# Kernel tuning notes

Hardware: AMD Instinct MI355X
Metric: run time of the kernel (lower is better)

## Reference

```python
import jax, jax.numpy as jnp
import numpy as np

N = 65536
EMB_DIM = 1024
PICK_NUM = 12  # ceil(ln(65536)) = ceil(11.09) = 12


def setup_inputs() -> dict:
    key = jax.random.key(0)
    k_emb, k_wq, k_bq, k_wk, k_bk, k_idx = jax.random.split(key, 6)
    s = 1.0 / np.sqrt(EMB_DIM)
    embed_matrix = jax.random.normal(k_emb, (N, EMB_DIM), dtype=jnp.float32)
    Wq = jax.random.normal(k_wq, (EMB_DIM, EMB_DIM), dtype=jnp.float32) * s
    bq = jax.random.normal(k_bq, (EMB_DIM,), dtype=jnp.float32) * s
    Wk = jax.random.normal(k_wk, (EMB_DIM, EMB_DIM), dtype=jnp.float32) * s
    bk = jax.random.normal(k_bk, (EMB_DIM,), dtype=jnp.float32) * s
    # np.random.choice(n, pick_num, replace=False) -> deterministic permutation slice
    indices = jax.random.permutation(k_idx, N)[:PICK_NUM].astype(jnp.int32)
    return {"embed_matrix": embed_matrix, "Wq": Wq, "bq": bq,
            "Wk": Wk, "bk": bk, "indices": indices}


def reference(embed_matrix, Wq, bq, Wk, bk, indices):
    pick_num = indices.shape[0]
    # torch.nn.Linear: y = x @ W.T + b
    query = embed_matrix @ Wq.T + bq          # [n, d]
    key = embed_matrix @ Wk.T + bk            # [n, d]
    new_key = key[indices]                    # [pick, d] sampled keys
    Q_K_sample = query @ new_key.T            # [n, pick]
    max_values = jnp.max(Q_K_sample, axis=1)  # [n]
    _, top_indices = jax.lax.top_k(max_values, pick_num)
    Q_reduced = query[top_indices]            # [pick, d]
    Q_K = Q_reduced @ key.T                   # [pick, n]
    pooled = jnp.max(Q_K, axis=0, keepdims=True)  # [1, n]
    attention_embed = pooled @ embed_matrix   # [1, d]
    return attention_embed
```

## Files before the change

### kernel.cpp

```cpp
#include <hip/hip_runtime.h>

#define DIM 1024
#define NROWS 65536
#define PICK 12


__global__ void __launch_bounds__(256)
rows12_kernel(const float* __restrict__ emb, const float* __restrict__ W,
              const float* __restrict__ b, const int* __restrict__ idx,
              float* __restrict__ out) {
    int d = blockIdx.x;
    int t = threadIdx.x;
    int lane = t & 63;
    int q = t >> 6;
    int e0 = q * 256 + lane * 4;
    float4 w4 = *(const float4*)&W[(size_t)d * DIM + e0];
    float part[PICK];
#pragma unroll
    for (int j = 0; j < PICK; ++j) {
        int r = idx[j];
        float4 e4 = *(const float4*)&emb[(size_t)r * DIM + e0];
        part[j] = w4.x * e4.x + w4.y * e4.y + w4.z * e4.z + w4.w * e4.w;
    }
#pragma unroll
    for (int j = 0; j < PICK; ++j) {
        float v = part[j];
        for (int s = 32; s > 0; s >>= 1) v += __shfl_down(v, s, 64);
        part[j] = v;
    }
    __shared__ float red[4][PICK];
    if (lane == 0) {
#pragma unroll
        for (int j = 0; j < PICK; ++j) red[q][j] = part[j];
    }
    __syncthreads();
    if (t < PICK) {
        float s = red[0][t] + red[1][t] + red[2][t] + red[3][t] + b[d];
        out[t * DIM + d] = s;
    }
}

__global__ void __launch_bounds__(256)
colmat_kernel(const float* __restrict__ W, const float* __restrict__ V,
              const float* __restrict__ b, float* __restrict__ out,
              float* __restrict__ cvec) {
    int blk = blockIdx.x;
    int t = threadIdx.x;
    if (blk == 128) {
        float part[PICK];
#pragma unroll
        for (int j = 0; j < PICK; ++j) part[j] = 0.f;
        for (int k = 0; k < 4; ++k) {
            int d = t + k * 256;
            float bv = b[d];
#pragma unroll
            for (int j = 0; j < PICK; ++j) part[j] += bv * V[j * DIM + d];
        }
#pragma unroll
        for (int j = 0; j < PICK; ++j) {
            float v = part[j];
            for (int s = 32; s > 0; s >>= 1) v += __shfl_down(v, s, 64);
            if ((t & 63) == 0) atomicAdd(&cvec[j], v);
        }
        return;
    }
    int eg = blk & 3;
    int dg = blk >> 2;
    int e = eg * 256 + t;
    int d0 = dg * 32;
    __shared__ float Vs[PICK][32];
    for (int i = t; i < PICK * 32; i += 256) {
        int j = i >> 5, dd = i & 31;
        Vs[j][dd] = V[j * DIM + d0 + dd];
    }
    __syncthreads();
    float acc[PICK];
#pragma unroll
    for (int j = 0; j < PICK; ++j) acc[j] = 0.f;
    for (int dd = 0; dd < 32; ++dd) {
        float w = W[(size_t)(d0 + dd) * DIM + e];
#pragma unroll
        for (int j = 0; j < PICK; ++j) acc[j] += w * Vs[j][dd];
    }
#pragma unroll
    for (int j = 0; j < PICK; ++j) atomicAdd(&out[e * PICK + j], acc[j]);
}


__global__ void __launch_bounds__(256)
pass1_kernel(const float* __restrict__ emb, const float* __restrict__ M,
             const float* __restrict__ c0, float* __restrict__ maxv) {
    __shared__ float sM[DIM * PICK];
    int t = threadIdx.x;
    for (int i = t; i < DIM * PICK / 4; i += 256)
        ((float4*)sM)[i] = ((const float4*)M)[i];
    __syncthreads();

    int l = t & 63, w = t >> 6;
    int g = l >> 2, s = l & 3;
    size_t wbase = (size_t)blockIdx.x * 256 + w * 64;
    const float* rp[4];
    float4 cur[4];
#pragma unroll
    for (int rr = 0; rr < 4; ++rr) {
        rp[rr] = emb + (wbase + rr * 16 + g) * DIM + s * 4;
        cur[rr] = *(const float4*)rp[rr];
    }
    float cb[PICK];
#pragma unroll
    for (int j = 0; j < PICK; ++j) cb[j] = c0[j];

    float acc[4][PICK];
#pragma unroll
    for (int rr = 0; rr < 4; ++rr)
#pragma unroll
        for (int j = 0; j < PICK; ++j) acc[rr][j] = 0.f;

    for (int i = 0; i < 64; ++i) {
        int ip = (i + 1 < 64) ? i + 1 : i;
        float4 nxt[4];
#pragma unroll
        for (int rr = 0; rr < 4; ++rr) nxt[rr] = *(const float4*)(rp[rr] + ip * 16);
        const float* mb = sM + (size_t)(i * 16 + s * 4) * PICK;
        float4 m[12];
#pragma unroll
        for (int k = 0; k < 12; ++k) m[k] = *(const float4*)(mb + k * 4);
#pragma unroll
        for (int rr = 0; rr < 4; ++rr) {
            float f[4] = {cur[rr].x, cur[rr].y, cur[rr].z, cur[rr].w};
#pragma unroll
            for (int x = 0; x < 4; ++x) {
                float4 a0 = m[3 * x], a1 = m[3 * x + 1], a2 = m[3 * x + 2];
                acc[rr][0] += f[x] * a0.x; acc[rr][1] += f[x] * a0.y;
                acc[rr][2] += f[x] * a0.z; acc[rr][3] += f[x] * a0.w;
                acc[rr][4] += f[x] * a1.x; acc[rr][5] += f[x] * a1.y;
                acc[rr][6] += f[x] * a1.z; acc[rr][7] += f[x] * a1.w;
                acc[rr][8] += f[x] * a2.x; acc[rr][9] += f[x] * a2.y;
                acc[rr][10] += f[x] * a2.z; acc[rr][11] += f[x] * a2.w;
            }
        }
#pragma unroll
        for (int rr = 0; rr < 4; ++rr) cur[rr] = nxt[rr];
    }
#pragma unroll
    for (int rr = 0; rr < 4; ++rr)
#pragma unroll
        for (int j = 0; j < PICK; ++j) {
            acc[rr][j] += __shfl_xor(acc[rr][j], 1, 64);
            acc[rr][j] += __shfl_xor(acc[rr][j], 2, 64);
        }
    float mx[4];
#pragma unroll
    for (int rr = 0; rr < 4; ++rr) {
        float v = acc[rr][0] + cb[0];
#pragma unroll
        for (int j = 1; j < PICK; ++j) v = fmaxf(v, acc[rr][j] + cb[j]);
        mx[rr] = v;
    }
    float sel = (s == 0) ? mx[0] : (s == 1) ? mx[1] : (s == 2) ? mx[2] : mx[3];
    maxv[wbase + s * 16 + g] = sel;
}

__global__ void __launch_bounds__(256)
pass2_kernel(const float* __restrict__ emb, const float* __restrict__ Rt,
             const float* __restrict__ c1, float* __restrict__ out) {
    __shared__ float sM[DIM * PICK];
    __shared__ float pooled[256];
    int t = threadIdx.x;
    for (int i = t; i < DIM * PICK / 4; i += 256)
        ((float4*)sM)[i] = ((const float4*)Rt)[i];
    __syncthreads();

    int l = t & 63, w = t >> 6;
    int g = l >> 2, s = l & 3;
    size_t bbase = (size_t)blockIdx.x * 256;
    size_t wbase = bbase + w * 64;
    const float* rp[4];
    float4 cur[4];
#pragma unroll
    for (int rr = 0; rr < 4; ++rr) {
        rp[rr] = emb + (wbase + rr * 16 + g) * DIM + s * 4;
        cur[rr] = *(const float4*)rp[rr];
    }
    float cb[PICK];
#pragma unroll
    for (int j = 0; j < PICK; ++j) cb[j] = c1[j];

    float acc[4][PICK];
#pragma unroll
    for (int rr = 0; rr < 4; ++rr)
#pragma unroll
        for (int j = 0; j < PICK; ++j) acc[rr][j] = 0.f;

    for (int i = 0; i < 64; ++i) {
        int ip = (i + 1 < 64) ? i + 1 : i;
        float4 nxt[4];
#pragma unroll
        for (int rr = 0; rr < 4; ++rr) nxt[rr] = *(const float4*)(rp[rr] + ip * 16);
        const float* mb = sM + (size_t)(i * 16 + s * 4) * PICK;
        float4 m[12];
#pragma unroll
        for (int k = 0; k < 12; ++k) m[k] = *(const float4*)(mb + k * 4);
#pragma unroll
        for (int rr = 0; rr < 4; ++rr) {
            float f[4] = {cur[rr].x, cur[rr].y, cur[rr].z, cur[rr].w};
#pragma unroll
            for (int x = 0; x < 4; ++x) {
                float4 a0 = m[3 * x], a1 = m[3 * x + 1], a2 = m[3 * x + 2];
                acc[rr][0] += f[x] * a0.x; acc[rr][1] += f[x] * a0.y;
                acc[rr][2] += f[x] * a0.z; acc[rr][3] += f[x] * a0.w;
                acc[rr][4] += f[x] * a1.x; acc[rr][5] += f[x] * a1.y;
                acc[rr][6] += f[x] * a1.z; acc[rr][7] += f[x] * a1.w;
                acc[rr][8] += f[x] * a2.x; acc[rr][9] += f[x] * a2.y;
                acc[rr][10] += f[x] * a2.z; acc[rr][11] += f[x] * a2.w;
            }
        }
#pragma unroll
        for (int rr = 0; rr < 4; ++rr) cur[rr] = nxt[rr];
    }
#pragma unroll
    for (int rr = 0; rr < 4; ++rr)
#pragma unroll
        for (int j = 0; j < PICK; ++j) {
            acc[rr][j] += __shfl_xor(acc[rr][j], 1, 64);
            acc[rr][j] += __shfl_xor(acc[rr][j], 2, 64);
        }
    float mx[4];
#pragma unroll
    for (int rr = 0; rr < 4; ++rr) {
        float v = acc[rr][0] + cb[0];
#pragma unroll
        for (int j = 1; j < PICK; ++j) v = fmaxf(v, acc[rr][j] + cb[j]);
        mx[rr] = v;
    }
    float sel = (s == 0) ? mx[0] : (s == 1) ? mx[1] : (s == 2) ? mx[2] : mx[3];
    pooled[w * 64 + s * 16 + g] = sel;
    __syncthreads();

    const float* tp = emb + bbase * DIM + t * 4;
    float4 o = {0.f, 0.f, 0.f, 0.f};
#pragma unroll 8
    for (int r = 0; r < 256; ++r) {
        float p = pooled[r];
        float4 v = *(const float4*)(tp + (size_t)r * DIM);
        o.x += p * v.x; o.y += p * v.y; o.z += p * v.z; o.w += p * v.w;
    }
    atomicAdd(&out[t * 4 + 0], o.x);
    atomicAdd(&out[t * 4 + 1], o.y);
    atomicAdd(&out[t * 4 + 2], o.z);
    atomicAdd(&out[t * 4 + 3], o.w);
}

__global__ void __launch_bounds__(256)
top12_local(const float* __restrict__ maxv, float* __restrict__ cand_v,
            int* __restrict__ cand_i) {
    int t = threadIdx.x;
    int base = blockIdx.x * 1024;
    __shared__ float mv[1024];
    __shared__ float sv[256];
    __shared__ int si[256];
    for (int i = t; i < 1024; i += 256) mv[i] = maxv[base + i];
    __syncthreads();
    for (int k = 0; k < PICK; ++k) {
        float bv = -3e38f; int bi = 0x7fffffff;
        for (int i = t; i < 1024; i += 256) {
            float v = mv[i];
            if (v > bv || (v == bv && base + i < bi)) { bv = v; bi = base + i; }
        }
        sv[t] = bv; si[t] = bi;
        __syncthreads();
        for (int s = 128; s > 0; s >>= 1) {
            if (t < s) {
                if (sv[t + s] > sv[t] || (sv[t + s] == sv[t] && si[t + s] < si[t])) {
                    sv[t] = sv[t + s]; si[t] = si[t + s];
                }
            }
            __syncthreads();
        }
        if (t == 0) {
            cand_v[blockIdx.x * PICK + k] = sv[0];
            cand_i[blockIdx.x * PICK + k] = si[0];
            mv[si[0] - base] = -3e38f;
        }
        __syncthreads();
    }
}

__global__ void __launch_bounds__(256)
top12_merge(const float* __restrict__ cand_v, const int* __restrict__ cand_i,
            int* __restrict__ top_idx) {
    int t = threadIdx.x;
    __shared__ float mv[768];
    __shared__ int mi[768];
    __shared__ float sv[256];
    __shared__ int si[256];
    __shared__ int sl[256];
    for (int i = t; i < 768; i += 256) { mv[i] = cand_v[i]; mi[i] = cand_i[i]; }
    __syncthreads();
    for (int k = 0; k < PICK; ++k) {
        float bv = -3e38f; int bi = 0x7fffffff; int bl = -1;
        for (int i = t; i < 768; i += 256) {
            float v = mv[i]; int ii = mi[i];
            if (v > bv || (v == bv && ii < bi)) { bv = v; bi = ii; bl = i; }
        }
        sv[t] = bv; si[t] = bi; sl[t] = bl;
        __syncthreads();
        for (int s = 128; s > 0; s >>= 1) {
            if (t < s) {
                if (sv[t + s] > sv[t] || (sv[t + s] == sv[t] && si[t + s] < si[t])) {
                    sv[t] = sv[t + s]; si[t] = si[t + s]; sl[t] = sl[t + s];
                }
            }
            __syncthreads();
        }
        if (t == 0) { top_idx[k] = si[0]; mv[sl[0]] = -3e38f; }
        __syncthreads();
    }
}

extern "C" void kernel_launch(void* const* d_in, const int* in_sizes, int n_in,
                              void* d_out, int out_size, void* d_ws, size_t ws_size,
                              hipStream_t stream) {
    const float* emb = (const float*)d_in[0];
    const float* Wq  = (const float*)d_in[1];
    const float* bq  = (const float*)d_in[2];
    const float* Wk  = (const float*)d_in[3];
    const float* bk  = (const float*)d_in[4];
    const int* indices = (const int*)d_in[5];
    float* out = (float*)d_out;
    float* ws = (float*)d_ws;

    float* NK      = ws;
    float* Qr      = ws + 12288;
    float* M       = ws + 24576;
    float* Rt      = ws + 36864;
    float* c0      = ws + 49152;
    float* c1      = ws + 49168;
    float* cand_v  = ws + 49184;
    int*   cand_i  = (int*)(ws + 49952);
    int*   top_idx = (int*)(ws + 50720);
    float* maxv    = ws + 50736;

    hipMemsetAsync(M, 0, (size_t)(12288 * 2 + 32) * sizeof(float), stream);
    hipMemsetAsync(out, 0, DIM * sizeof(float), stream);

    rows12_kernel<<<1024, 256, 0, stream>>>(emb, Wk, bk, indices, NK);
    colmat_kernel<<<129, 256, 0, stream>>>(Wq, NK, bq, M, c0);
    pass1_kernel<<<256, 256, 0, stream>>>(emb, M, c0, maxv);
    top12_local<<<64, 256, 0, stream>>>(maxv, cand_v, cand_i);
    top12_merge<<<1, 256, 0, stream>>>(cand_v, cand_i, top_idx);
    rows12_kernel<<<1024, 256, 0, stream>>>(emb, Wq, bq, top_idx, Qr);
    colmat_kernel<<<129, 256, 0, stream>>>(Wk, Qr, bk, Rt, c1);
    pass2_kernel<<<256, 256, 0, stream>>>(emb, Rt, c1, out);
}
```

Baseline: 605.9 us.

## Halve rows per block in streaming passes, deepen prefetch, use wave-level top-k

pass1 and pass2 now give each block 128 rows instead of 256, launch twice as many blocks, and request two resident blocks per CU. They also prefetch two iterations ahead instead of one. The aim is to spread the 256 MB embedding stream over all CUs, since 256 blocks underfills a 256-CU part, and to hide more memory latency. The top-12 local and merge kernels are rewritten as single-wavefront register and shuffle reductions, which removes the shared-memory tree and its barriers. The cost is more per-block shared-memory reloads of the 48 KB matrix and twice as many output atomics in pass2.

```diff
diff --git a/kernel.cpp b/kernel.cpp
--- a/kernel.cpp
+++ b/kernel.cpp
@@ -87,7 +87,7 @@
 }
 
 
-__global__ void __launch_bounds__(256)
+__global__ void __launch_bounds__(256, 2)
 pass1_kernel(const float* __restrict__ emb, const float* __restrict__ M,
              const float* __restrict__ c0, float* __restrict__ maxv) {
     __shared__ float sM[DIM * PICK];
@@ -98,35 +98,36 @@
 
     int l = t & 63, w = t >> 6;
     int g = l >> 2, s = l & 3;
-    size_t wbase = (size_t)blockIdx.x * 256 + w * 64;
-    const float* rp[4];
-    float4 cur[4];
-#pragma unroll
-    for (int rr = 0; rr < 4; ++rr) {
+    size_t wbase = (size_t)blockIdx.x * 128 + w * 32;
+    const float* rp[2];
+    float4 cur[2], nxt[2];
+#pragma unroll
+    for (int rr = 0; rr < 2; ++rr) {
         rp[rr] = emb + (wbase + rr * 16 + g) * DIM + s * 4;
         cur[rr] = *(const float4*)rp[rr];
+        nxt[rr] = *(const float4*)(rp[rr] + 16);
     }
     float cb[PICK];
 #pragma unroll
     for (int j = 0; j < PICK; ++j) cb[j] = c0[j];
 
-    float acc[4][PICK];
-#pragma unroll
-    for (int rr = 0; rr < 4; ++rr)
+    float acc[2][PICK];
+#pragma unroll
+    for (int rr = 0; rr < 2; ++rr)
 #pragma unroll
         for (int j = 0; j < PICK; ++j) acc[rr][j] = 0.f;
 
     for (int i = 0; i < 64; ++i) {
-        int ip = (i + 1 < 64) ? i + 1 : i;
-        float4 nxt[4];
-#pragma unroll
-        for (int rr = 0; rr < 4; ++rr) nxt[rr] = *(const float4*)(rp[rr] + ip * 16);
+        int ip2 = (i + 2 < 64) ? i + 2 : 63;
+        float4 n2[2];
+#pragma unroll
+        for (int rr = 0; rr < 2; ++rr) n2[rr] = *(const float4*)(rp[rr] + ip2 * 16);
         const float* mb = sM + (size_t)(i * 16 + s * 4) * PICK;
         float4 m[12];
 #pragma unroll
         for (int k = 0; k < 12; ++k) m[k] = *(const float4*)(mb + k * 4);
 #pragma unroll
-        for (int rr = 0; rr < 4; ++rr) {
+        for (int rr = 0; rr < 2; ++rr) {
             float f[4] = {cur[rr].x, cur[rr].y, cur[rr].z, cur[rr].w};
 #pragma unroll
             for (int x = 0; x < 4; ++x) {
@@ -140,32 +141,31 @@
             }
         }
 #pragma unroll
-        for (int rr = 0; rr < 4; ++rr) cur[rr] = nxt[rr];
-    }
-#pragma unroll
-    for (int rr = 0; rr < 4; ++rr)
+        for (int rr = 0; rr < 2; ++rr) { cur[rr] = nxt[rr]; nxt[rr] = n2[rr]; }
+    }
+#pragma unroll
+    for (int rr = 0; rr < 2; ++rr)
 #pragma unroll
         for (int j = 0; j < PICK; ++j) {
             acc[rr][j] += __shfl_xor(acc[rr][j], 1, 64);
             acc[rr][j] += __shfl_xor(acc[rr][j], 2, 64);
         }
-    float mx[4];
-#pragma unroll
-    for (int rr = 0; rr < 4; ++rr) {
+    float mx[2];
+#pragma unroll
+    for (int rr = 0; rr < 2; ++rr) {
         float v = acc[rr][0] + cb[0];
 #pragma unroll
         for (int j = 1; j < PICK; ++j) v = fmaxf(v, acc[rr][j] + cb[j]);
         mx[rr] = v;
     }
-    float sel = (s == 0) ? mx[0] : (s == 1) ? mx[1] : (s == 2) ? mx[2] : mx[3];
-    maxv[wbase + s * 16 + g] = sel;
-}
-
-__global__ void __launch_bounds__(256)
+    if (s < 2) maxv[wbase + s * 16 + g] = (s == 0) ? mx[0] : mx[1];
+}
+
+__global__ void __launch_bounds__(256, 2)
 pass2_kernel(const float* __restrict__ emb, const float* __restrict__ Rt,
              const float* __restrict__ c1, float* __restrict__ out) {
     __shared__ float sM[DIM * PICK];
-    __shared__ float pooled[256];
+    __shared__ float pooled[128];
     int t = threadIdx.x;
     for (int i = t; i < DIM * PICK / 4; i += 256)
         ((float4*)sM)[i] = ((const float4*)Rt)[i];
@@ -173,36 +173,37 @@
 
     int l = t & 63, w = t >> 6;
     int g = l >> 2, s = l & 3;
-    size_t bbase = (size_t)blockIdx.x * 256;
-    size_t wbase = bbase + w * 64;
-    const float* rp[4];
-    float4 cur[4];
-#pragma unroll
-    for (int rr = 0; rr < 4; ++rr) {
+    size_t bbase = (size_t)blockIdx.x * 128;
+    size_t wbase = bbase + w * 32;
+    const float* rp[2];
+    float4 cur[2], nxt[2];
+#pragma unroll
+    for (int rr = 0; rr < 2; ++rr) {
         rp[rr] = emb + (wbase + rr * 16 + g) * DIM + s * 4;
         cur[rr] = *(const float4*)rp[rr];
+        nxt[rr] = *(const float4*)(rp[rr] + 16);
     }
     float cb[PICK];
 #pragma unroll
     for (int j = 0; j < PICK; ++j) cb[j] = c1[j];
 
-    float acc[4][PICK];
-#pragma unroll
-    for (int rr = 0; rr < 4; ++rr)
+    float acc[2][PICK];
+#pragma unroll
+    for (int rr = 0; rr < 2; ++rr)
 #pragma unroll
         for (int j = 0; j < PICK; ++j) acc[rr][j] = 0.f;
 
     for (int i = 0; i < 64; ++i) {
-        int ip = (i + 1 < 64) ? i + 1 : i;
-        float4 nxt[4];
-#pragma unroll
-        for (int rr = 0; rr < 4; ++rr) nxt[rr] = *(const float4*)(rp[rr] + ip * 16);
+        int ip2 = (i + 2 < 64) ? i + 2 : 63;
+        float4 n2[2];
+#pragma unroll
+        for (int rr = 0; rr < 2; ++rr) n2[rr] = *(const float4*)(rp[rr] + ip2 * 16);
         const float* mb = sM + (size_t)(i * 16 + s * 4) * PICK;
         float4 m[12];
 #pragma unroll
         for (int k = 0; k < 12; ++k) m[k] = *(const float4*)(mb + k * 4);
 #pragma unroll
-        for (int rr = 0; rr < 4; ++rr) {
+        for (int rr = 0; rr < 2; ++rr) {
             float f[4] = {cur[rr].x, cur[rr].y, cur[rr].z, cur[rr].w};
 #pragma unroll
             for (int x = 0; x < 4; ++x) {
@@ -216,31 +217,30 @@
             }
         }
 #pragma unroll
-        for (int rr = 0; rr < 4; ++rr) cur[rr] = nxt[rr];
-    }
-#pragma unroll
-    for (int rr = 0; rr < 4; ++rr)
+        for (int rr = 0; rr < 2; ++rr) { cur[rr] = nxt[rr]; nxt[rr] = n2[rr]; }
+    }
+#pragma unroll
+    for (int rr = 0; rr < 2; ++rr)
 #pragma unroll
         for (int j = 0; j < PICK; ++j) {
             acc[rr][j] += __shfl_xor(acc[rr][j], 1, 64);
             acc[rr][j] += __shfl_xor(acc[rr][j], 2, 64);
         }
-    float mx[4];
-#pragma unroll
-    for (int rr = 0; rr < 4; ++rr) {
+    float mx[2];
+#pragma unroll
+    for (int rr = 0; rr < 2; ++rr) {
         float v = acc[rr][0] + cb[0];
 #pragma unroll
         for (int j = 1; j < PICK; ++j) v = fmaxf(v, acc[rr][j] + cb[j]);
         mx[rr] = v;
     }
-    float sel = (s == 0) ? mx[0] : (s == 1) ? mx[1] : (s == 2) ? mx[2] : mx[3];
-    pooled[w * 64 + s * 16 + g] = sel;
+    if (s < 2) pooled[w * 32 + s * 16 + g] = (s == 0) ? mx[0] : mx[1];
     __syncthreads();
 
     const float* tp = emb + bbase * DIM + t * 4;
     float4 o = {0.f, 0.f, 0.f, 0.f};
 #pragma unroll 8
-    for (int r = 0; r < 256; ++r) {
+    for (int r = 0; r < 128; ++r) {
         float p = pooled[r];
         float4 v = *(const float4*)(tp + (size_t)r * DIM);
         o.x += p * v.x; o.y += p * v.y; o.z += p * v.z; o.w += p * v.w;
@@ -251,70 +251,67 @@
     atomicAdd(&out[t * 4 + 3], o.w);
 }
 
-__global__ void __launch_bounds__(256)
+__global__ void __launch_bounds__(64)
 top12_local(const float* __restrict__ maxv, float* __restrict__ cand_v,
             int* __restrict__ cand_i) {
     int t = threadIdx.x;
     int base = blockIdx.x * 1024;
-    __shared__ float mv[1024];
-    __shared__ float sv[256];
-    __shared__ int si[256];
-    for (int i = t; i < 1024; i += 256) mv[i] = maxv[base + i];
-    __syncthreads();
+    float lv[16];
+#pragma unroll
+    for (int q = 0; q < 16; ++q) lv[q] = maxv[base + q * 64 + t];
     for (int k = 0; k < PICK; ++k) {
         float bv = -3e38f; int bi = 0x7fffffff;
-        for (int i = t; i < 1024; i += 256) {
-            float v = mv[i];
-            if (v > bv || (v == bv && base + i < bi)) { bv = v; bi = base + i; }
-        }
-        sv[t] = bv; si[t] = bi;
-        __syncthreads();
-        for (int s = 128; s > 0; s >>= 1) {
-            if (t < s) {
-                if (sv[t + s] > sv[t] || (sv[t + s] == sv[t] && si[t + s] < si[t])) {
-                    sv[t] = sv[t + s]; si[t] = si[t + s];
-                }
-            }
-            __syncthreads();
+#pragma unroll
+        for (int q = 0; q < 16; ++q) {
+            int ii = base + q * 64 + t;
+            float v = lv[q];
+            if (v > bv || (v == bv && ii < bi)) { bv = v; bi = ii; }
+        }
+#pragma unroll
+        for (int sft = 1; sft < 64; sft <<= 1) {
+            float ov = __shfl_xor(bv, sft, 64);
+            int oi = __shfl_xor(bi, sft, 64);
+            if (ov > bv || (ov == bv && oi < bi)) { bv = ov; bi = oi; }
         }
         if (t == 0) {
-            cand_v[blockIdx.x * PICK + k] = sv[0];
-            cand_i[blockIdx.x * PICK + k] = si[0];
-            mv[si[0] - base] = -3e38f;
-        }
-        __syncthreads();
-    }
-}
-
-__global__ void __launch_bounds__(256)
+            cand_v[blockIdx.x * PICK + k] = bv;
+            cand_i[blockIdx.x * PICK + k] = bi;
+        }
+#pragma unroll
+        for (int q = 0; q < 16; ++q)
+            if (base + q * 64 + t == bi) lv[q] = -3e38f;
+    }
+}
+
+__global__ void __launch_bounds__(64)
 top12_merge(const float* __restrict__ cand_v, const int* __restrict__ cand_i,
             int* __restrict__ top_idx) {
     int t = threadIdx.x;
-    __shared__ float mv[768];
-    __shared__ int mi[768];
-    __shared__ float sv[256];
-    __shared__ int si[256];
-    __shared__ int sl[256];
-    for (int i = t; i < 768; i += 256) { mv[i] = cand_v[i]; mi[i] = cand_i[i]; }
-    __syncthreads();
+    float lv[12]; int li[12];
+#pragma unroll
+    for (int q = 0; q < 12; ++q) {
+        lv[q] = cand_v[q * 64 + t];
+        li[q] = cand_i[q * 64 + t];
+    }
     for (int k = 0; k < PICK; ++k) {
-        float bv = -3e38f; int bi = 0x7fffffff; int bl = -1;
-        for (int i = t; i < 768; i += 256) {
-            float v = mv[i]; int ii = mi[i];
-            if (v > bv || (v == bv && ii < bi)) { bv = v; bi = ii; bl = i; }
-        }
-        sv[t] = bv; si[t] = bi; sl[t] = bl;
-        __syncthreads();
-        for (int s = 128; s > 0; s >>= 1) {
-            if (t < s) {
-                if (sv[t + s] > sv[t] || (sv[t + s] == sv[t] && si[t + s] < si[t])) {
-                    sv[t] = sv[t + s]; si[t] = si[t + s]; sl[t] = sl[t + s];
-                }
+        float bv = -3e38f; int bi = 0x7fffffff; int bs = -1;
+#pragma unroll
+        for (int q = 0; q < 12; ++q) {
+            if (lv[q] > bv || (lv[q] == bv && li[q] < bi)) {
+                bv = lv[q]; bi = li[q]; bs = q * 64 + t;
             }
-            __syncthreads();
-        }
-        if (t == 0) { top_idx[k] = si[0]; mv[sl[0]] = -3e38f; }
-        __syncthreads();
+        }
+#pragma unroll
+        for (int sft = 1; sft < 64; sft <<= 1) {
+            float ov = __shfl_xor(bv, sft, 64);
+            int oi = __shfl_xor(bi, sft, 64);
+            int os = __shfl_xor(bs, sft, 64);
+            if (ov > bv || (ov == bv && oi < bi)) { bv = ov; bi = oi; bs = os; }
+        }
+        if (t == 0) top_idx[k] = bi;
+#pragma unroll
+        for (int q = 0; q < 12; ++q)
+            if (q * 64 + t == bs) lv[q] = -3e38f;
     }
 }
 
@@ -346,10 +343,10 @@
 
     rows12_kernel<<<1024, 256, 0, stream>>>(emb, Wk, bk, indices, NK);
     colmat_kernel<<<129, 256, 0, stream>>>(Wq, NK, bq, M, c0);
-    pass1_kernel<<<256, 256, 0, stream>>>(emb, M, c0, maxv);
-    top12_local<<<64, 256, 0, stream>>>(maxv, cand_v, cand_i);
-    top12_merge<<<1, 256, 0, stream>>>(cand_v, cand_i, top_idx);
+    pass1_kernel<<<512, 256, 0, stream>>>(emb, M, c0, maxv);
+    top12_local<<<64, 64, 0, stream>>>(maxv, cand_v, cand_i);
+    top12_merge<<<1, 64, 0, stream>>>(cand_v, cand_i, top_idx);
     rows12_kernel<<<1024, 256, 0, stream>>>(emb, Wq, bq, top_idx, Qr);
     colmat_kernel<<<129, 256, 0, stream>>>(Wk, Qr, bk, Rt, c1);
-    pass2_kernel<<<256, 256, 0, stream>>>(emb, Rt, c1, out);
-}
+    pass2_kernel<<<512, 256, 0, stream>>>(emb, Rt, c1, out);
+}
```

New measurement: 700.9 us. 1.16x slower.
